# Performance work log

Hardware: AMD Instinct MI355X
Metric: run time of the kernel (lower is better)

## Reference

```python
import jax, jax.numpy as jnp
import numpy as np

N = 100000
E = 1600000
IN_CH = 64
HID = 32


def _gatv2(x, src, dst, wl, bl, wr, br, att, bias, heads, out_ch, concat):
    # GATv2Conv (PyG semantics, share_weights=False, negative_slope=0.2,
    # self-loops already appended to src/dst by caller).
    n = x.shape[0]
    xl = (x @ wl + bl).reshape(n, heads, out_ch)  # source transform
    xr = (x @ wr + br).reshape(n, heads, out_ch)  # target transform
    xj = xl[src]                                   # [E, H, C]
    xi = xr[dst]
    e = jax.nn.leaky_relu(xi + xj, negative_slope=0.2)
    alpha = jnp.einsum('ehc,hc->eh', e, att)       # [E, H]
    amax = jax.ops.segment_max(alpha, dst, num_segments=n)
    alpha = jnp.exp(alpha - amax[dst])
    denom = jax.ops.segment_sum(alpha, dst, num_segments=n)
    alpha = alpha / (denom[dst] + 1e-16)
    out = jax.ops.segment_sum(alpha[:, :, None] * xj, dst, num_segments=n)
    out = out.reshape(n, heads * out_ch) if concat else out.mean(axis=1)
    return out + bias


def setup_inputs() -> dict:
    key = jax.random.key(0)
    ks = jax.random.split(key, 20)
    s = 0.1
    d = {
        'x': jax.random.normal(ks[0], (N, IN_CH), jnp.float32),
        'edge_index': jax.random.randint(ks[1], (2, E), 0, N, jnp.int32),
        # conv1: in=64 -> heads=4, C=32, concat
        'w1l': s * jax.random.normal(ks[2], (IN_CH, 4 * HID), jnp.float32),
        'b1l': jnp.zeros((4 * HID,), jnp.float32),
        'w1r': s * jax.random.normal(ks[3], (IN_CH, 4 * HID), jnp.float32),
        'b1r': jnp.zeros((4 * HID,), jnp.float32),
        'a1': s * jax.random.normal(ks[4], (4, HID), jnp.float32),
        'c1': jnp.zeros((4 * HID,), jnp.float32),
        # conv2: in=128 -> heads=2, C=32, concat
        'w2l': s * jax.random.normal(ks[5], (4 * HID, 2 * HID), jnp.float32),
        'b2l': jnp.zeros((2 * HID,), jnp.float32),
        'w2r': s * jax.random.normal(ks[6], (4 * HID, 2 * HID), jnp.float32),
        'b2r': jnp.zeros((2 * HID,), jnp.float32),
        'a2': s * jax.random.normal(ks[7], (2, HID), jnp.float32),
        'c2': jnp.zeros((2 * HID,), jnp.float32),
        # conv3: in=64 -> heads=1, C=32, mean (concat=False)
        'w3l': s * jax.random.normal(ks[8], (2 * HID, HID), jnp.float32),
        'b3l': jnp.zeros((HID,), jnp.float32),
        'w3r': s * jax.random.normal(ks[9], (2 * HID, HID), jnp.float32),
        'b3r': jnp.zeros((HID,), jnp.float32),
        'a3': s * jax.random.normal(ks[10], (1, HID), jnp.float32),
        'c3': jnp.zeros((HID,), jnp.float32),
        # MLP head 32 -> 16 -> 2
        'wm1': s * jax.random.normal(ks[11], (HID, HID // 2), jnp.float32),
        'bm1': jnp.zeros((HID // 2,), jnp.float32),
        'wm2': s * jax.random.normal(ks[12], (HID // 2, 2), jnp.float32),
        'bm2': jnp.zeros((2,), jnp.float32),
    }
    return d


def reference(x, edge_index,
              w1l, b1l, w1r, b1r, a1, c1,
              w2l, b2l, w2r, b2r, a2, c2,
              w3l, b3l, w3r, b3r, a3, c3,
              wm1, bm1, wm2, bm2):
    n = x.shape[0]
    loop = jnp.arange(n, dtype=edge_index.dtype)
    src = jnp.concatenate([edge_index[0], loop])  # add_self_loops=True (PyG default)
    dst = jnp.concatenate([edge_index[1], loop])
    h = jax.nn.relu(_gatv2(x, src, dst, w1l, b1l, w1r, b1r, a1, c1, 4, HID, True))
    h = jax.nn.relu(_gatv2(h, src, dst, w2l, b2l, w2r, b2r, a2, c2, 2, HID, True))
    h = jax.nn.relu(_gatv2(h, src, dst, w3l, b3l, w3r, b3r, a3, c3, 1, HID, False))
    raw = jax.nn.relu(h @ wm1 + bm1) @ wm2 + bm2
    v_mag = jax.nn.sigmoid(raw[:, 0]) + 0.5
    v_angle = jnp.tanh(raw[:, 1]) * 180.0
    return jnp.stack([v_mag, v_angle], axis=1)
```

## Files before the change

### kernel.cpp

```cpp
#include <hip/hip_runtime.h>
#include <hip/hip_fp16.h>


constexpr int N = 100000;
constexpr int E = 1600000;
constexpr int S = 48;

constexpr int NBUK = (N + 127) >> 7;
constexpr int BCAP = 384;
constexpr int EPB = 8192;
constexpr int BIN_B = (E + EPB - 1) / EPB;
constexpr int XMM_B = (N + 63) / 64;

typedef _Float16 half8_t __attribute__((ext_vector_type(8)));
typedef _Float16 half4_t __attribute__((ext_vector_type(4)));
typedef _Float16 h2 __attribute__((ext_vector_type(2)));
typedef float f32x4 __attribute__((ext_vector_type(4)));


__global__ __launch_bounds__(256) void k_bin(const int* __restrict__ ei,
                                             int* __restrict__ bcnt,
                                             unsigned* __restrict__ bbuf) {
  __shared__ int hist[NBUK];
  const int tid = threadIdx.x;
  const int cls = blockIdx.x & 7;
  const int e0 = blockIdx.x * EPB;
  for (int i = tid; i < NBUK; i += 256) hist[i] = 0;
  __syncthreads();
  #pragma unroll 4
  for (int j = 0; j < EPB / 256; ++j) {
    const int e = e0 + j * 256 + tid;
    if (e < E) atomicAdd(&hist[ei[E + e] >> 7], 1);
  }
  __syncthreads();
  for (int i = tid; i < NBUK; i += 256) {
    const int h = hist[i];
    hist[i] = h ? atomicAdd(&bcnt[i * 8 + cls], h) : 0;
  }
  __syncthreads();
  #pragma unroll 4
  for (int j = 0; j < EPB / 256; ++j) {
    const int e = e0 + j * 256 + tid;
    if (e < E) {
      const int src = ei[e];
      const int dst = ei[E + e];
      const int b = dst >> 7;
      const int pos = atomicAdd(&hist[b], 1);
      if (pos < BCAP)
        bbuf[(size_t)(b * 8 + cls) * BCAP + pos] =
            ((unsigned)(dst & 127) << 17) | (unsigned)src;
    }
  }
}


__global__ __launch_bounds__(256) void k_insert(const int* __restrict__ bcnt,
                                                const unsigned* __restrict__ bbuf,
                                                int* __restrict__ deg,
                                                int* __restrict__ ebuf) {
  __shared__ int cnt[128];
  const int b = blockIdx.x;
  const int tid = threadIdx.x;
  const int node0 = b * 128 + tid;
  if (tid < 128) {
    cnt[tid] = 1;
    if (node0 < N) ebuf[node0 * S] = node0;
  }
  __syncthreads();
  #pragma unroll 1
  for (int c = 0; c < 8; ++c) {
    const int n = min(bcnt[b * 8 + c], BCAP);
    const unsigned* arr = bbuf + (size_t)(b * 8 + c) * BCAP;
    for (int i = tid; i < n; i += 256) {
      const unsigned ent = arr[i];
      const int dlo = (int)(ent >> 17);
      const int src = (int)(ent & 0x1FFFFu);
      const int pos = atomicAdd(&cnt[dlo], 1);
      if (pos < S) ebuf[(b * 128 + dlo) * S + pos] = src;
    }
  }
  __syncthreads();
  if (tid < 128 && node0 < N) deg[node0] = cnt[tid];
}


template <int K, int M>
__device__ __forceinline__ void wprep_body(const float* __restrict__ src,
                                           __half* __restrict__ dst, int blk) {
  const int idx = blk * 256 + threadIdx.x;
  const int k = idx / M;
  const int m = idx % M;
  ((_Float16*)dst)[m * K + (k ^ ((m & 7) << 3))] = (_Float16)src[idx];
}

__global__ __launch_bounds__(256) void k_wprep(
    const float* w1l, const float* w1r, const float* w2l, const float* w2r,
    const float* w3l, const float* w3r,
    __half* o1l, __half* o1r, __half* o2l, __half* o2r,
    __half* o3l, __half* o3r) {
  int b = blockIdx.x;
  if      (b < 32)  wprep_body<64, 128>(w1l, o1l, b);
  else if (b < 64)  wprep_body<64, 128>(w1r, o1r, b - 32);
  else if (b < 96)  wprep_body<128, 64>(w2l, o2l, b - 64);
  else if (b < 128) wprep_body<128, 64>(w2r, o2r, b - 96);
  else if (b < 136) wprep_body<64, 32>(w3l, o3l, b - 128);
  else              wprep_body<64, 32>(w3r, o3r, b - 136);
}


template <int K, int M>
__global__ __launch_bounds__(256) void k_xmm(const float* __restrict__ x,
                                             const __half* __restrict__ wtl,
                                             const __half* __restrict__ wtr,
                                             const float* __restrict__ bl,
                                             const float* __restrict__ br,
                                             __half* __restrict__ Aout,
                                             __half* __restrict__ Bout) {
  constexpr int XSZ = 64 * K;
  constexpr int WSZ = M * K;
  constexpr int KS = K / 32;
  constexpr int CT = M / 16;
  __shared__ _Float16 pool[XSZ + 2 * WSZ];

  const int tid = threadIdx.x;
  const int node0 = blockIdx.x * 64;

  for (int i = tid; i < 64 * (K / 4); i += 256) {
    const int row = i / (K / 4);
    const int c4 = i % (K / 4);
    const int grow = min(node0 + row, N - 1);
    float4 v = reinterpret_cast<const float4*>(x)[(size_t)grow * (K / 4) + c4];
    const int k0 = c4 * 4;
    const int hidx = row * K + ((k0) ^ ((row & 7) << 3));
    *reinterpret_cast<half4_t*>(&pool[hidx]) =
        (half4_t){(_Float16)v.x, (_Float16)v.y, (_Float16)v.z, (_Float16)v.w};
  }
  for (int i = tid; i < WSZ / 8; i += 256) {
    reinterpret_cast<uint4*>(&pool[XSZ])[i] =
        reinterpret_cast<const uint4*>(wtl)[i];
    reinterpret_cast<uint4*>(&pool[XSZ + WSZ])[i] =
        reinterpret_cast<const uint4*>(wtr)[i];
  }
  __syncthreads();

  const int lane = tid & 63;
  const int wid = tid >> 6;
  const int r0 = wid * 16;

  half8_t af[KS];
  #pragma unroll
  for (int ks = 0; ks < KS; ++ks) {
    const int row = r0 + (lane & 15);
    const int k0 = ks * 32 + (lane >> 4) * 8;
    af[ks] = *reinterpret_cast<const half8_t*>(
        &pool[row * K + (k0 ^ ((row & 7) << 3))]);
  }

  f32x4 accl[CT], accr[CT];
  #pragma unroll
  for (int ct = 0; ct < CT; ++ct) {
    accl[ct] = (f32x4){0.f, 0.f, 0.f, 0.f};
    accr[ct] = (f32x4){0.f, 0.f, 0.f, 0.f};
  }

  #pragma unroll
  for (int ct = 0; ct < CT; ++ct) {
    #pragma unroll
    for (int ks = 0; ks < KS; ++ks) {
      const int col = ct * 16 + (lane & 15);
      const int k0 = ks * 32 + (lane >> 4) * 8;
      const int hb = col * K + (k0 ^ ((col & 7) << 3));
      half8_t bfl = *reinterpret_cast<const half8_t*>(&pool[XSZ + hb]);
      accl[ct] = __builtin_amdgcn_mfma_f32_16x16x32_f16(af[ks], bfl, accl[ct], 0, 0, 0);
      half8_t bfr = *reinterpret_cast<const half8_t*>(&pool[XSZ + WSZ + hb]);
      accr[ct] = __builtin_amdgcn_mfma_f32_16x16x32_f16(af[ks], bfr, accr[ct], 0, 0, 0);
    }
  }

  __syncthreads();
  #pragma unroll
  for (int ct = 0; ct < CT; ++ct) {
    const int col = ct * 16 + (lane & 15);
    const float bb = bl[col];
    #pragma unroll
    for (int r = 0; r < 4; ++r) {
      const int row = r0 + (lane >> 4) * 4 + r;
      pool[row * M + col] = (_Float16)(accl[ct][r] + bb);
    }
  }
  __syncthreads();
  for (int i = tid; i < 64 * (M / 8); i += 256) {
    const int row = i / (M / 8);
    const int j = i % (M / 8);
    const int g = node0 + row;
    if (g < N)
      reinterpret_cast<uint4*>(Aout + (size_t)g * M)[j] =
          reinterpret_cast<uint4*>(&pool[row * M])[j];
  }
  __syncthreads();
  #pragma unroll
  for (int ct = 0; ct < CT; ++ct) {
    const int col = ct * 16 + (lane & 15);
    const float bb = br[col];
    #pragma unroll
    for (int r = 0; r < 4; ++r) {
      const int row = r0 + (lane >> 4) * 4 + r;
      pool[row * M + col] = (_Float16)(accr[ct][r] + bb);
    }
  }
  __syncthreads();
  for (int i = tid; i < 64 * (M / 8); i += 256) {
    const int row = i / (M / 8);
    const int j = i % (M / 8);
    const int g = node0 + row;
    if (g < N)
      reinterpret_cast<uint4*>(Bout + (size_t)g * M)[j] =
          reinterpret_cast<uint4*>(&pool[row * M])[j];
  }
}


template <int CTRL>
__device__ __forceinline__ float dpp_add(float x) {
  return x + __builtin_bit_cast(float,
      __builtin_amdgcn_update_dpp(0, __builtin_bit_cast(int, x),
                                  CTRL, 0xF, 0xF, true));
}

template <int H>
__global__ __launch_bounds__(256) void k_gat(const __half* __restrict__ xl,
                                             const __half* __restrict__ xr,
                                             const float* __restrict__ att,
                                             const float* __restrict__ bias,
                                             const int* __restrict__ deg,
                                             const int* __restrict__ ebuf,
                                             float* __restrict__ out) {
  constexpr int F = H * 32;
  constexpr int F8 = F / 8;
  constexpr int F4 = F / 4;
  constexpr int LPE = F8;
  constexpr int EPI = 64 / LPE;
  constexpr float LOG2E = 1.44269504088896f;
  const int lane = threadIdx.x & 63;
  const int node = (blockIdx.x * blockDim.x + threadIdx.x) >> 6;
  if (node >= N) return;
  const int li = lane & (LPE - 1);
  const int eg = lane / LPE;

  const uint4* xl4 = reinterpret_cast<const uint4*>(xl);
  const uint4* xr4 = reinterpret_cast<const uint4*>(xr);

  const uint4 xiraw = xr4[(unsigned)node * F8 + li];
  h2 xi2[4];
  xi2[0] = __builtin_bit_cast(h2, xiraw.x);
  xi2[1] = __builtin_bit_cast(h2, xiraw.y);
  xi2[2] = __builtin_bit_cast(h2, xiraw.z);
  xi2[3] = __builtin_bit_cast(h2, xiraw.w);

  const float4 at0 = reinterpret_cast<const float4*>(att)[li * 2];
  const float4 at1 = reinterpret_cast<const float4*>(att)[li * 2 + 1];
  h2 at2[4];
  at2[0] = (h2){(_Float16)(at0.x * LOG2E), (_Float16)(at0.y * LOG2E)};
  at2[1] = (h2){(_Float16)(at0.z * LOG2E), (_Float16)(at0.w * LOG2E)};
  at2[2] = (h2){(_Float16)(at1.x * LOG2E), (_Float16)(at1.y * LOG2E)};
  at2[3] = (h2){(_Float16)(at1.z * LOG2E), (_Float16)(at1.w * LOG2E)};
  const h2 c02 = {(_Float16)0.2f, (_Float16)0.2f};

  float4 acc0 = make_float4(0.f, 0.f, 0.f, 0.f);
  float4 acc1 = make_float4(0.f, 0.f, 0.f, 0.f);
  float l = 0.f;

  const int* row = ebuf + node * S;
  const int dn = min(deg[node], S);
  const int last = dn - 1;
  const int iters = (dn + EPI - 1) / EPI;

  auto process = [&](const uint4& raw, bool valid) {
    h2 xj0 = __builtin_bit_cast(h2, raw.x);
    h2 xj1 = __builtin_bit_cast(h2, raw.y);
    h2 xj2 = __builtin_bit_cast(h2, raw.z);
    h2 xj3 = __builtin_bit_cast(h2, raw.w);
    float t = 0.f;
    h2 v;
    v = xi2[0] + xj0; v = __builtin_elementwise_max(v, v * c02);
    t = __builtin_amdgcn_fdot2(at2[0], v, t, false);
    v = xi2[1] + xj1; v = __builtin_elementwise_max(v, v * c02);
    t = __builtin_amdgcn_fdot2(at2[1], v, t, false);
    v = xi2[2] + xj2; v = __builtin_elementwise_max(v, v * c02);
    t = __builtin_amdgcn_fdot2(at2[2], v, t, false);
    v = xi2[3] + xj3; v = __builtin_elementwise_max(v, v * c02);
    t = __builtin_amdgcn_fdot2(at2[3], v, t, false);
    t = dpp_add<0xB1>(t);
    t = dpp_add<0x4E>(t);
    float pm = valid ? exp2f(t) : 0.f;
    l += pm;
    acc0.x = fmaf(pm, (float)xj0[0], acc0.x);
    acc0.y = fmaf(pm, (float)xj0[1], acc0.y);
    acc0.z = fmaf(pm, (float)xj1[0], acc0.z);
    acc0.w = fmaf(pm, (float)xj1[1], acc0.w);
    acc1.x = fmaf(pm, (float)xj2[0], acc1.x);
    acc1.y = fmaf(pm, (float)xj2[1], acc1.y);
    acc1.z = fmaf(pm, (float)xj3[0], acc1.z);
    acc1.w = fmaf(pm, (float)xj3[1], acc1.w);
  };

  int i = eg;
  bool vA = i < dn;
  int s0 = row[min(i, last)];
  i += EPI;
  uint4 xjA = xl4[(unsigned)s0 * F8 + li];
  bool vB = i < dn;
  int sN = row[min(i, last)];
  i += EPI;
  uint4 xjB;

  for (int it = 0; it < iters; it += 2) {
    xjB = xl4[(unsigned)sN * F8 + li];
    bool vn = i < dn;
    sN = row[min(i, last)];
    i += EPI;
    process(xjA, vA);
    vA = vn;
    xjA = xl4[(unsigned)sN * F8 + li];
    vn = i < dn;
    sN = row[min(i, last)];
    i += EPI;
    process(xjB, vB);
    vB = vn;
  }

  #pragma unroll
  for (int ofs = LPE; ofs < 64; ofs <<= 1) {
    acc0.x += __shfl_xor(acc0.x, ofs);
    acc0.y += __shfl_xor(acc0.y, ofs);
    acc0.z += __shfl_xor(acc0.z, ofs);
    acc0.w += __shfl_xor(acc0.w, ofs);
    acc1.x += __shfl_xor(acc1.x, ofs);
    acc1.y += __shfl_xor(acc1.y, ofs);
    acc1.z += __shfl_xor(acc1.z, ofs);
    acc1.w += __shfl_xor(acc1.w, ofs);
    l      += __shfl_xor(l, ofs);
  }

  if (lane < LPE) {
    const float inv = 1.f / (l + 1e-16f);
    const float4 bv0 = reinterpret_cast<const float4*>(bias)[li * 2];
    const float4 bv1 = reinterpret_cast<const float4*>(bias)[li * 2 + 1];
    float4 r0, r1;
    r0.x = fmaxf(acc0.x * inv + bv0.x, 0.f);
    r0.y = fmaxf(acc0.y * inv + bv0.y, 0.f);
    r0.z = fmaxf(acc0.z * inv + bv0.z, 0.f);
    r0.w = fmaxf(acc0.w * inv + bv0.w, 0.f);
    r1.x = fmaxf(acc1.x * inv + bv1.x, 0.f);
    r1.y = fmaxf(acc1.y * inv + bv1.y, 0.f);
    r1.z = fmaxf(acc1.z * inv + bv1.z, 0.f);
    r1.w = fmaxf(acc1.w * inv + bv1.w, 0.f);
    float4* op = reinterpret_cast<float4*>(out) + (unsigned)node * F4 + li * 2;
    op[0] = r0;
    op[1] = r1;
  }
}


__global__ __launch_bounds__(256) void k_mlp(const float* __restrict__ h,
                                             const float* __restrict__ wm1,
                                             const float* __restrict__ bm1,
                                             const float* __restrict__ wm2,
                                             const float* __restrict__ bm2,
                                             float* __restrict__ out) {
  __shared__ float w1[512], b1[16], w2[32], b2[2];
  const int tid = threadIdx.x;
  for (int i = tid; i < 512; i += 256) w1[i] = wm1[i];
  if (tid < 16) b1[tid] = bm1[tid];
  if (tid < 32) w2[tid] = wm2[tid];
  if (tid < 2)  b2[tid] = bm2[tid];
  __syncthreads();
  const int node = blockIdx.x * blockDim.x + tid;
  if (node >= N) return;
  float hv[32];
  const float* hp = h + (size_t)node * 32;
  #pragma unroll
  for (int k = 0; k < 8; ++k) {
    float4 v = reinterpret_cast<const float4*>(hp)[k];
    hv[4 * k] = v.x; hv[4 * k + 1] = v.y; hv[4 * k + 2] = v.z; hv[4 * k + 3] = v.w;
  }
  float r0 = b2[0], r1 = b2[1];
  #pragma unroll
  for (int j = 0; j < 16; ++j) {
    float a = b1[j];
    #pragma unroll
    for (int k = 0; k < 32; ++k) a += hv[k] * w1[k * 16 + j];
    a = fmaxf(a, 0.f);
    r0 += a * w2[j * 2];
    r1 += a * w2[j * 2 + 1];
  }
  float vm = 1.f / (1.f + __expf(-r0)) + 0.5f;
  float va = tanhf(r1) * 180.f;
  out[(size_t)node * 2]     = vm;
  out[(size_t)node * 2 + 1] = va;
}


extern "C" void kernel_launch(void* const* d_in, const int* in_sizes, int n_in,
                              void* d_out, int out_size, void* d_ws, size_t ws_size,
                              hipStream_t stream) {
  const float* x   = (const float*)d_in[0];
  const int*   ei  = (const int*)d_in[1];
  const float* w1l = (const float*)d_in[2];
  const float* b1l = (const float*)d_in[3];
  const float* w1r = (const float*)d_in[4];
  const float* b1r = (const float*)d_in[5];
  const float* a1  = (const float*)d_in[6];
  const float* c1  = (const float*)d_in[7];
  const float* w2l = (const float*)d_in[8];
  const float* b2l = (const float*)d_in[9];
  const float* w2r = (const float*)d_in[10];
  const float* b2r = (const float*)d_in[11];
  const float* a2  = (const float*)d_in[12];
  const float* c2  = (const float*)d_in[13];
  const float* w3l = (const float*)d_in[14];
  const float* b3l = (const float*)d_in[15];
  const float* w3r = (const float*)d_in[16];
  const float* b3r = (const float*)d_in[17];
  const float* a3  = (const float*)d_in[18];
  const float* c3  = (const float*)d_in[19];
  const float* wm1 = (const float*)d_in[20];
  const float* bm1 = (const float*)d_in[21];
  const float* wm2 = (const float*)d_in[22];
  const float* bm2 = (const float*)d_in[23];
  float* outp = (float*)d_out;
  (void)in_sizes; (void)n_in; (void)out_size; (void)ws_size;

  char* ws = (char*)d_ws;
  size_t o = 0;
  auto take = [&](size_t bytes) {
    char* p = ws + o;
    o = (o + bytes + 255) & ~(size_t)255;
    return p;
  };
  int* deg       = (int*)take((size_t)N * sizeof(int));
  int* ebuf      = (int*)take((size_t)N * S * sizeof(int));
  int* bcnt      = (int*)take((size_t)NBUK * 8 * sizeof(int));
  unsigned* bbuf = (unsigned*)take((size_t)NBUK * 8 * BCAP * sizeof(unsigned));
  __half* A      = (__half*)take((size_t)N * 128 * sizeof(__half));
  __half* B      = (__half*)take((size_t)N * 128 * sizeof(__half));
  float* Cb      = (float*)take((size_t)N * 128 * sizeof(float));
  __half* t1l    = (__half*)take(128 * 64 * sizeof(__half));
  __half* t1r    = (__half*)take(128 * 64 * sizeof(__half));
  __half* t2l    = (__half*)take(64 * 128 * sizeof(__half));
  __half* t2r    = (__half*)take(64 * 128 * sizeof(__half));
  __half* t3l    = (__half*)take(32 * 64 * sizeof(__half));
  __half* t3r    = (__half*)take(32 * 64 * sizeof(__half));

  hipMemsetAsync(bcnt, 0, (size_t)NBUK * 8 * sizeof(int), stream);
  k_wprep<<<144, 256, 0, stream>>>(w1l, w1r, w2l, w2r, w3l, w3r,
                                   t1l, t1r, t2l, t2r, t3l, t3r);
  k_bin<<<BIN_B, 256, 0, stream>>>(ei, bcnt, bbuf);
  k_insert<<<NBUK, 256, 0, stream>>>(bcnt, bbuf, deg, ebuf);

  k_xmm<64, 128><<<XMM_B, 256, 0, stream>>>(x, t1l, t1r, b1l, b1r, A, B);
  k_gat<4><<<N / 4, 256, 0, stream>>>(A, B, a1, c1, deg, ebuf, Cb);

  k_xmm<128, 64><<<XMM_B, 256, 0, stream>>>(Cb, t2l, t2r, b2l, b2r, A, B);
  k_gat<2><<<N / 4, 256, 0, stream>>>(A, B, a2, c2, deg, ebuf, Cb);

  k_xmm<64, 32><<<XMM_B, 256, 0, stream>>>(Cb, t3l, t3r, b3l, b3r, A, B);
  k_gat<1><<<N / 4, 256, 0, stream>>>(A, B, a3, c3, deg, ebuf, Cb);

  k_mlp<<<(N + 255) / 256, 256, 0, stream>>>(Cb, wm1, bm1, wm2, bm2, outp);
}
```

Baseline: 392.6 us.

## Store GAT layer outputs in fp16 and widen per-lane channel width for layer one

Intermediate per-node activations between GAT layers are now written in fp16 instead of fp32. The following matmul loads them directly without conversion, and the MLP reads fp16. The first GAT layer gives each lane 16 channels, so more edges are processed per wave. The edge-loop prefetch is restructured, and the binning kernel handles twice as many edges per block. Together these aim to cut intermediate memory traffic and raise edge parallelism, at the cost of extra fp16 rounding in the activations.

```diff
diff --git a/kernel.cpp b/kernel.cpp
--- a/kernel.cpp
+++ b/kernel.cpp
@@ -8,7 +8,7 @@
 
 constexpr int NBUK = (N + 127) >> 7;
 constexpr int BCAP = 384;
-constexpr int EPB = 8192;
+constexpr int EPB = 16384;
 constexpr int BIN_B = (E + EPB - 1) / EPB;
 constexpr int XMM_B = (N + 63) / 64;
 
@@ -108,8 +108,8 @@
 }
 
 
-template <int K, int M>
-__global__ __launch_bounds__(256) void k_xmm(const float* __restrict__ x,
+template <int K, int M, bool FP16IN>
+__global__ __launch_bounds__(256) void k_xmm(const void* __restrict__ xin,
                                              const __half* __restrict__ wtl,
                                              const __half* __restrict__ wtr,
                                              const float* __restrict__ bl,
@@ -125,15 +125,28 @@
   const int tid = threadIdx.x;
   const int node0 = blockIdx.x * 64;
 
-  for (int i = tid; i < 64 * (K / 4); i += 256) {
-    const int row = i / (K / 4);
-    const int c4 = i % (K / 4);
-    const int grow = min(node0 + row, N - 1);
-    float4 v = reinterpret_cast<const float4*>(x)[(size_t)grow * (K / 4) + c4];
-    const int k0 = c4 * 4;
-    const int hidx = row * K + ((k0) ^ ((row & 7) << 3));
-    *reinterpret_cast<half4_t*>(&pool[hidx]) =
-        (half4_t){(_Float16)v.x, (_Float16)v.y, (_Float16)v.z, (_Float16)v.w};
+  if constexpr (!FP16IN) {
+    const float* x = (const float*)xin;
+    for (int i = tid; i < 64 * (K / 4); i += 256) {
+      const int row = i / (K / 4);
+      const int c4 = i % (K / 4);
+      const int grow = min(node0 + row, N - 1);
+      float4 v = reinterpret_cast<const float4*>(x)[(size_t)grow * (K / 4) + c4];
+      const int k0 = c4 * 4;
+      const int hidx = row * K + (k0 ^ ((row & 7) << 3));
+      *reinterpret_cast<half4_t*>(&pool[hidx]) =
+          (half4_t){(_Float16)v.x, (_Float16)v.y, (_Float16)v.z, (_Float16)v.w};
+    }
+  } else {
+    const uint4* x = (const uint4*)xin;
+    for (int i = tid; i < 64 * (K / 8); i += 256) {
+      const int row = i / (K / 8);
+      const int c8 = i % (K / 8);
+      const int grow = min(node0 + row, N - 1);
+      uint4 v = x[(size_t)grow * (K / 8) + c8];
+      const int k0 = c8 * 8;
+      *reinterpret_cast<uint4*>(&pool[row * K + (k0 ^ ((row & 7) << 3))]) = v;
+    }
   }
   for (int i = tid; i < WSZ / 8; i += 256) {
     reinterpret_cast<uint4*>(&pool[XSZ])[i] =
@@ -227,18 +240,19 @@
                                   CTRL, 0xF, 0xF, true));
 }
 
-template <int H>
+template <int H, int CPL>
 __global__ __launch_bounds__(256) void k_gat(const __half* __restrict__ xl,
                                              const __half* __restrict__ xr,
                                              const float* __restrict__ att,
                                              const float* __restrict__ bias,
                                              const int* __restrict__ deg,
                                              const int* __restrict__ ebuf,
-                                             float* __restrict__ out) {
+                                             __half* __restrict__ out) {
   constexpr int F = H * 32;
   constexpr int F8 = F / 8;
-  constexpr int F4 = F / 4;
-  constexpr int LPE = F8;
+  constexpr int C8 = CPL / 8;
+  constexpr int QH = CPL / 2;
+  constexpr int LPE = F / CPL;
   constexpr int EPI = 64 / LPE;
   constexpr float LOG2E = 1.44269504088896f;
   const int lane = threadIdx.x & 63;
@@ -249,25 +263,29 @@
 
   const uint4* xl4 = reinterpret_cast<const uint4*>(xl);
   const uint4* xr4 = reinterpret_cast<const uint4*>(xr);
-
-  const uint4 xiraw = xr4[(unsigned)node * F8 + li];
-  h2 xi2[4];
-  xi2[0] = __builtin_bit_cast(h2, xiraw.x);
-  xi2[1] = __builtin_bit_cast(h2, xiraw.y);
-  xi2[2] = __builtin_bit_cast(h2, xiraw.z);
-  xi2[3] = __builtin_bit_cast(h2, xiraw.w);
-
-  const float4 at0 = reinterpret_cast<const float4*>(att)[li * 2];
-  const float4 at1 = reinterpret_cast<const float4*>(att)[li * 2 + 1];
-  h2 at2[4];
-  at2[0] = (h2){(_Float16)(at0.x * LOG2E), (_Float16)(at0.y * LOG2E)};
-  at2[1] = (h2){(_Float16)(at0.z * LOG2E), (_Float16)(at0.w * LOG2E)};
-  at2[2] = (h2){(_Float16)(at1.x * LOG2E), (_Float16)(at1.y * LOG2E)};
-  at2[3] = (h2){(_Float16)(at1.z * LOG2E), (_Float16)(at1.w * LOG2E)};
+  const unsigned base = (unsigned)node * F8 + li * C8;
+
+  h2 xi2[QH];
+  #pragma unroll
+  for (int c = 0; c < C8; ++c) {
+    const uint4 r = xr4[base + c];
+    xi2[c * 4 + 0] = __builtin_bit_cast(h2, r.x);
+    xi2[c * 4 + 1] = __builtin_bit_cast(h2, r.y);
+    xi2[c * 4 + 2] = __builtin_bit_cast(h2, r.z);
+    xi2[c * 4 + 3] = __builtin_bit_cast(h2, r.w);
+  }
+  h2 at2[QH];
+  #pragma unroll
+  for (int q = 0; q < CPL / 4; ++q) {
+    const float4 a = reinterpret_cast<const float4*>(att)[li * (CPL / 4) + q];
+    at2[2 * q]     = (h2){(_Float16)(a.x * LOG2E), (_Float16)(a.y * LOG2E)};
+    at2[2 * q + 1] = (h2){(_Float16)(a.z * LOG2E), (_Float16)(a.w * LOG2E)};
+  }
   const h2 c02 = {(_Float16)0.2f, (_Float16)0.2f};
 
-  float4 acc0 = make_float4(0.f, 0.f, 0.f, 0.f);
-  float4 acc1 = make_float4(0.f, 0.f, 0.f, 0.f);
+  float acc[CPL];
+  #pragma unroll
+  for (int k = 0; k < CPL; ++k) acc[k] = 0.f;
   float l = 0.f;
 
   const int* row = ebuf + node * S;
@@ -275,94 +293,93 @@
   const int last = dn - 1;
   const int iters = (dn + EPI - 1) / EPI;
 
-  auto process = [&](const uint4& raw, bool valid) {
-    h2 xj0 = __builtin_bit_cast(h2, raw.x);
-    h2 xj1 = __builtin_bit_cast(h2, raw.y);
-    h2 xj2 = __builtin_bit_cast(h2, raw.z);
-    h2 xj3 = __builtin_bit_cast(h2, raw.w);
+  auto process = [&](const uint4* raw, bool valid) {
+    h2 xj2[QH];
+    #pragma unroll
+    for (int c = 0; c < C8; ++c) {
+      xj2[c * 4 + 0] = __builtin_bit_cast(h2, raw[c].x);
+      xj2[c * 4 + 1] = __builtin_bit_cast(h2, raw[c].y);
+      xj2[c * 4 + 2] = __builtin_bit_cast(h2, raw[c].z);
+      xj2[c * 4 + 3] = __builtin_bit_cast(h2, raw[c].w);
+    }
     float t = 0.f;
-    h2 v;
-    v = xi2[0] + xj0; v = __builtin_elementwise_max(v, v * c02);
-    t = __builtin_amdgcn_fdot2(at2[0], v, t, false);
-    v = xi2[1] + xj1; v = __builtin_elementwise_max(v, v * c02);
-    t = __builtin_amdgcn_fdot2(at2[1], v, t, false);
-    v = xi2[2] + xj2; v = __builtin_elementwise_max(v, v * c02);
-    t = __builtin_amdgcn_fdot2(at2[2], v, t, false);
-    v = xi2[3] + xj3; v = __builtin_elementwise_max(v, v * c02);
-    t = __builtin_amdgcn_fdot2(at2[3], v, t, false);
+    #pragma unroll
+    for (int q = 0; q < QH; ++q) {
+      h2 v = xi2[q] + xj2[q];
+      v = __builtin_elementwise_max(v, v * c02);
+      t = __builtin_amdgcn_fdot2(at2[q], v, t, false);
+    }
     t = dpp_add<0xB1>(t);
-    t = dpp_add<0x4E>(t);
+    if constexpr (CPL == 8) t = dpp_add<0x4E>(t);
     float pm = valid ? exp2f(t) : 0.f;
     l += pm;
-    acc0.x = fmaf(pm, (float)xj0[0], acc0.x);
-    acc0.y = fmaf(pm, (float)xj0[1], acc0.y);
-    acc0.z = fmaf(pm, (float)xj1[0], acc0.z);
-    acc0.w = fmaf(pm, (float)xj1[1], acc0.w);
-    acc1.x = fmaf(pm, (float)xj2[0], acc1.x);
-    acc1.y = fmaf(pm, (float)xj2[1], acc1.y);
-    acc1.z = fmaf(pm, (float)xj3[0], acc1.z);
-    acc1.w = fmaf(pm, (float)xj3[1], acc1.w);
+    #pragma unroll
+    for (int q = 0; q < QH; ++q) {
+      acc[2 * q]     = fmaf(pm, (float)xj2[q][0], acc[2 * q]);
+      acc[2 * q + 1] = fmaf(pm, (float)xj2[q][1], acc[2 * q + 1]);
+    }
   };
 
   int i = eg;
-  bool vA = i < dn;
+  bool v0 = i < dn;
   int s0 = row[min(i, last)];
   i += EPI;
-  uint4 xjA = xl4[(unsigned)s0 * F8 + li];
-  bool vB = i < dn;
-  int sN = row[min(i, last)];
+  bool v1 = i < dn;
+  int s1 = row[min(i, last)];
   i += EPI;
-  uint4 xjB;
-
-  for (int it = 0; it < iters; it += 2) {
-    xjB = xl4[(unsigned)sN * F8 + li];
-    bool vn = i < dn;
-    sN = row[min(i, last)];
+  uint4 x0[C8];
+  #pragma unroll
+  for (int c = 0; c < C8; ++c) x0[c] = xl4[(unsigned)s0 * F8 + li * C8 + c];
+
+  #pragma unroll 2
+  for (int it = 0; it < iters; ++it) {
+    uint4 x1[C8];
+    #pragma unroll
+    for (int c = 0; c < C8; ++c) x1[c] = xl4[(unsigned)s1 * F8 + li * C8 + c];
+    const bool v2 = i < dn;
+    const int s2 = row[min(i, last)];
     i += EPI;
-    process(xjA, vA);
-    vA = vn;
-    xjA = xl4[(unsigned)sN * F8 + li];
-    vn = i < dn;
-    sN = row[min(i, last)];
-    i += EPI;
-    process(xjB, vB);
-    vB = vn;
+    process(x0, v0);
+    #pragma unroll
+    for (int c = 0; c < C8; ++c) x0[c] = x1[c];
+    s1 = s2; v0 = v1; v1 = v2;
   }
 
   #pragma unroll
   for (int ofs = LPE; ofs < 64; ofs <<= 1) {
-    acc0.x += __shfl_xor(acc0.x, ofs);
-    acc0.y += __shfl_xor(acc0.y, ofs);
-    acc0.z += __shfl_xor(acc0.z, ofs);
-    acc0.w += __shfl_xor(acc0.w, ofs);
-    acc1.x += __shfl_xor(acc1.x, ofs);
-    acc1.y += __shfl_xor(acc1.y, ofs);
-    acc1.z += __shfl_xor(acc1.z, ofs);
-    acc1.w += __shfl_xor(acc1.w, ofs);
-    l      += __shfl_xor(l, ofs);
+    #pragma unroll
+    for (int k = 0; k < CPL; ++k) acc[k] += __shfl_xor(acc[k], ofs);
+    l += __shfl_xor(l, ofs);
   }
 
   if (lane < LPE) {
     const float inv = 1.f / (l + 1e-16f);
-    const float4 bv0 = reinterpret_cast<const float4*>(bias)[li * 2];
-    const float4 bv1 = reinterpret_cast<const float4*>(bias)[li * 2 + 1];
-    float4 r0, r1;
-    r0.x = fmaxf(acc0.x * inv + bv0.x, 0.f);
-    r0.y = fmaxf(acc0.y * inv + bv0.y, 0.f);
-    r0.z = fmaxf(acc0.z * inv + bv0.z, 0.f);
-    r0.w = fmaxf(acc0.w * inv + bv0.w, 0.f);
-    r1.x = fmaxf(acc1.x * inv + bv1.x, 0.f);
-    r1.y = fmaxf(acc1.y * inv + bv1.y, 0.f);
-    r1.z = fmaxf(acc1.z * inv + bv1.z, 0.f);
-    r1.w = fmaxf(acc1.w * inv + bv1.w, 0.f);
-    float4* op = reinterpret_cast<float4*>(out) + (unsigned)node * F4 + li * 2;
-    op[0] = r0;
-    op[1] = r1;
-  }
-}
-
-
-__global__ __launch_bounds__(256) void k_mlp(const float* __restrict__ h,
+    float bb[CPL];
+    #pragma unroll
+    for (int q = 0; q < CPL / 4; ++q) {
+      const float4 b4 = reinterpret_cast<const float4*>(bias)[li * (CPL / 4) + q];
+      bb[4 * q] = b4.x; bb[4 * q + 1] = b4.y;
+      bb[4 * q + 2] = b4.z; bb[4 * q + 3] = b4.w;
+    }
+    uint4* op = reinterpret_cast<uint4*>(out) + base;
+    #pragma unroll
+    for (int c = 0; c < C8; ++c) {
+      uint4 o;
+      #pragma unroll
+      for (int p = 0; p < 4; ++p) {
+        const int k = c * 8 + p * 2;
+        const float r0 = fmaxf(acc[k] * inv + bb[k], 0.f);
+        const float r1 = fmaxf(acc[k + 1] * inv + bb[k + 1], 0.f);
+        const h2 hh = {(_Float16)r0, (_Float16)r1};
+        (&o.x)[p] = __builtin_bit_cast(unsigned, hh);
+      }
+      op[c] = o;
+    }
+  }
+}
+
+
+__global__ __launch_bounds__(256) void k_mlp(const __half* __restrict__ h,
                                              const float* __restrict__ wm1,
                                              const float* __restrict__ bm1,
                                              const float* __restrict__ wm2,
@@ -378,11 +395,16 @@
   const int node = blockIdx.x * blockDim.x + tid;
   if (node >= N) return;
   float hv[32];
-  const float* hp = h + (size_t)node * 32;
-  #pragma unroll
-  for (int k = 0; k < 8; ++k) {
-    float4 v = reinterpret_cast<const float4*>(hp)[k];
-    hv[4 * k] = v.x; hv[4 * k + 1] = v.y; hv[4 * k + 2] = v.z; hv[4 * k + 3] = v.w;
+  const uint4* hp = reinterpret_cast<const uint4*>(h) + (size_t)node * 4;
+  #pragma unroll
+  for (int c = 0; c < 4; ++c) {
+    const uint4 r = hp[c];
+    #pragma unroll
+    for (int p = 0; p < 4; ++p) {
+      const h2 hh = __builtin_bit_cast(h2, (&r.x)[p]);
+      hv[c * 8 + p * 2]     = (float)hh[0];
+      hv[c * 8 + p * 2 + 1] = (float)hh[1];
+    }
   }
   float r0 = b2[0], r1 = b2[1];
   #pragma unroll
@@ -444,7 +466,7 @@
   unsigned* bbuf = (unsigned*)take((size_t)NBUK * 8 * BCAP * sizeof(unsigned));
   __half* A      = (__half*)take((size_t)N * 128 * sizeof(__half));
   __half* B      = (__half*)take((size_t)N * 128 * sizeof(__half));
-  float* Cb      = (float*)take((size_t)N * 128 * sizeof(float));
+  __half* Cb     = (__half*)take((size_t)N * 128 * sizeof(__half));
   __half* t1l    = (__half*)take(128 * 64 * sizeof(__half));
   __half* t1r    = (__half*)take(128 * 64 * sizeof(__half));
   __half* t2l    = (__half*)take(64 * 128 * sizeof(__half));
@@ -458,14 +480,14 @@
   k_bin<<<BIN_B, 256, 0, stream>>>(ei, bcnt, bbuf);
   k_insert<<<NBUK, 256, 0, stream>>>(bcnt, bbuf, deg, ebuf);
 
-  k_xmm<64, 128><<<XMM_B, 256, 0, stream>>>(x, t1l, t1r, b1l, b1r, A, B);
-  k_gat<4><<<N / 4, 256, 0, stream>>>(A, B, a1, c1, deg, ebuf, Cb);
-
-  k_xmm<128, 64><<<XMM_B, 256, 0, stream>>>(Cb, t2l, t2r, b2l, b2r, A, B);
-  k_gat<2><<<N / 4, 256, 0, stream>>>(A, B, a2, c2, deg, ebuf, Cb);
-
-  k_xmm<64, 32><<<XMM_B, 256, 0, stream>>>(Cb, t3l, t3r, b3l, b3r, A, B);
-  k_gat<1><<<N / 4, 256, 0, stream>>>(A, B, a3, c3, deg, ebuf, Cb);
+  k_xmm<64, 128, false><<<XMM_B, 256, 0, stream>>>(x, t1l, t1r, b1l, b1r, A, B);
+  k_gat<4, 16><<<N / 4, 256, 0, stream>>>(A, B, a1, c1, deg, ebuf, Cb);
+
+  k_xmm<128, 64, true><<<XMM_B, 256, 0, stream>>>(Cb, t2l, t2r, b2l, b2r, A, B);
+  k_gat<2, 8><<<N / 4, 256, 0, stream>>>(A, B, a2, c2, deg, ebuf, Cb);
+
+  k_xmm<64, 32, true><<<XMM_B, 256, 0, stream>>>(Cb, t3l, t3r, b3l, b3r, A, B);
+  k_gat<1, 8><<<N / 4, 256, 0, stream>>>(A, B, a3, c3, deg, ebuf, Cb);
 
   k_mlp<<<(N + 255) / 256, 256, 0, stream>>>(Cb, wm1, bm1, wm2, bm2, outp);
 }
```

Measured after the change: 430.5 us. 9.7% more time.
